# Kernel optimization log

Hardware: AMD Instinct MI355X
Metric: run time of the kernel (lower is better)

## Reference

```python
import jax, jax.numpy as jnp
import numpy as np

D_MODEL = 1024
N_HEADS = 16
D_HEAD = D_MODEL // N_HEADS
BLOCK = 2048
EPS = 1e-5


def layer_norm(x, w, b):
    mu = jnp.mean(x, axis=-1, keepdims=True)
    var = jnp.mean(jnp.square(x - mu), axis=-1, keepdims=True)
    return (x - mu) * jax.lax.rsqrt(var + EPS) * w + b


def setup_inputs() -> dict:
    key = jax.random.key(0)
    ks = jax.random.split(key, 8)
    d = D_MODEL
    s = 1.0 / np.sqrt(d)
    return {
        "x": jax.random.normal(ks[0], (2, 2048, d), dtype=jnp.float32),
        "ln1_w": jnp.ones((d,), jnp.float32),
        "ln1_b": jnp.zeros((d,), jnp.float32),
        "ln2_w": jnp.ones((d,), jnp.float32),
        "ln2_b": jnp.zeros((d,), jnp.float32),
        "qkv_w": jax.random.normal(ks[1], (3 * d, d), jnp.float32) * s,
        "o_w": jax.random.normal(ks[2], (d, d), jnp.float32) * s,
        "ffn_w1": jax.random.normal(ks[3], (4 * d, d), jnp.float32) * s,
        "ffn_b1": jnp.zeros((4 * d,), jnp.float32),
        "ffn_w2": jax.random.normal(ks[4], (d, 4 * d), jnp.float32) * (1.0 / np.sqrt(4 * d)),
        "ffn_b2": jnp.zeros((d,), jnp.float32),
    }


def reference(x, ln1_w, ln1_b, ln2_w, ln2_b, qkv_w, o_w, ffn_w1, ffn_b1, ffn_w2, ffn_b2):
    b, n, d = x.shape
    h = layer_norm(x, ln1_w, ln1_b)
    # qkv: (b, n, 3, H, Dh)
    qkv = (h @ qkv_w.T).reshape(b, n, 3, N_HEADS, D_HEAD)
    q, k, v = qkv[:, :, 0], qkv[:, :, 1], qkv[:, :, 2]  # (b, n, H, Dh)
    scale = 1.0 / np.sqrt(D_HEAD)
    s = jnp.einsum("bqhd,bkhd->bhqk", q, k) * scale
    mask = jnp.tril(jnp.ones((n, n), dtype=bool))
    s = jnp.where(mask, s, -jnp.inf)
    a = jax.nn.softmax(s, axis=-1)
    attn_out = jnp.einsum("bhqk,bkhd->bqhd", a, v).reshape(b, n, d)
    x = x + attn_out @ o_w.T
    h2 = layer_norm(x, ln2_w, ln2_b)
    ff = jax.nn.gelu(h2 @ ffn_w1.T + ffn_b1, approximate=False) @ ffn_w2.T + ffn_b2
    return x + ff
```

## Files before the change

kernel.cpp:

```cpp
#include <hip/hip_runtime.h>
#include <math.h>

#define D_MODEL 1024
#define N_HEADS 16
#define D_HEAD  64
#define SEQ     2048
#define BATCH   2
#define M_TOT   (BATCH*SEQ)
#define FFN_DIM 4096

typedef __attribute__((ext_vector_type(8))) short bf16x8;
typedef __attribute__((ext_vector_type(4))) float f32x4;
typedef __attribute__((ext_vector_type(8))) unsigned short u16x8;

__device__ __forceinline__ unsigned short f2bf(float f) {
  unsigned int u = __float_as_uint(f);
  return (unsigned short)((u + 0x7fffu + ((u >> 16) & 1u)) >> 16);
}
__device__ __forceinline__ unsigned short f2bf_trunc(float f) {
  return (unsigned short)(__float_as_uint(f) >> 16);
}
__device__ __forceinline__ float bf2f(unsigned short s) {
  return __uint_as_float(((unsigned int)s) << 16);
}

__device__ __forceinline__ void async_ld16(void* lds, const void* g) {
  __builtin_amdgcn_global_load_lds(
      (const __attribute__((address_space(1))) unsigned int*)g,
      (__attribute__((address_space(3))) unsigned int*)lds, 16, 0, 0);
}

__device__ __forceinline__ float gelu_exact(float x) {
  return 0.5f * x * (1.f + erff(x * 0.70710678118654752f));
}

__global__ __launch_bounds__(256) void cvt_all(const float* __restrict__ qkv_w,
    const float* __restrict__ o_w, const float* __restrict__ w1,
    const float* __restrict__ w2, unsigned short* __restrict__ dst) {
  const long MEGc = 1024*1024;
  long i = (long)(blockIdx.x*256 + threadIdx.x)*4;
  const float* src; long off;
  if (i < 3*MEGc)      { src = qkv_w; off = i; }
  else if (i < 4*MEGc) { src = o_w;  off = i - 3*MEGc; }
  else if (i < 8*MEGc) { src = w1;   off = i - 4*MEGc; }
  else                 { src = w2;   off = i - 8*MEGc; }
  float4 v = *(const float4*)(src + off);
  ushort4 o = { f2bf(v.x), f2bf(v.y), f2bf(v.z), f2bf(v.w) };
  *(ushort4*)(dst + i) = o;
}

__global__ __launch_bounds__(256) void ln_kernel(const float* __restrict__ x,
    const float* __restrict__ w, const float* __restrict__ b,
    unsigned short* __restrict__ out) {
  int row = blockIdx.x;
  const float* xr = x + (size_t)row * D_MODEL;
  int c = threadIdx.x * 4;
  float4 v = *(const float4*)(xr + c);
  float s = v.x + v.y + v.z + v.w;
  __shared__ float red[4];
  #pragma unroll
  for (int o = 32; o > 0; o >>= 1) s += __shfl_down(s, o, 64);
  int wave = threadIdx.x >> 6;
  if ((threadIdx.x & 63) == 0) red[wave] = s;
  __syncthreads();
  float mean = (red[0]+red[1]+red[2]+red[3]) * (1.f/D_MODEL);
  __syncthreads();
  float d0 = v.x-mean, d1 = v.y-mean, d2 = v.z-mean, d3 = v.w-mean;
  float s2 = d0*d0 + d1*d1 + d2*d2 + d3*d3;
  #pragma unroll
  for (int o = 32; o > 0; o >>= 1) s2 += __shfl_down(s2, o, 64);
  if ((threadIdx.x & 63) == 0) red[wave] = s2;
  __syncthreads();
  float var = (red[0]+red[1]+red[2]+red[3]) * (1.f/D_MODEL);
  float rs = rsqrtf(var + 1e-5f);
  float4 wv = *(const float4*)(w + c);
  float4 bv = *(const float4*)(b + c);
  ushort4 o = { f2bf(d0*rs*wv.x + bv.x), f2bf(d1*rs*wv.y + bv.y),
                f2bf(d2*rs*wv.z + bv.z), f2bf(d3*rs*wv.w + bv.w) };
  *(ushort4*)(out + (size_t)row*D_MODEL + c) = o;
}

__device__ __forceinline__ void swizzle_block(int nbx, int nby, int& bx, int& by) {
  int nb = nbx * nby;
  int bid = blockIdx.y * nbx + blockIdx.x;
  int chunk = nb >> 3;
  int bid2 = (bid & 7) * chunk + (bid >> 3);
  const int GM = 8;
  int ngroup = GM * nbx;
  int g = bid2 / ngroup, rem = bid2 % ngroup;
  by = g*GM + (rem % GM);
  bx = rem / GM;
}

template<int EPI, bool OBF, int BN>
__global__ __launch_bounds__(256) void gemm_mfma(
    const unsigned short* __restrict__ A, const unsigned short* __restrict__ Bt,
    float* __restrict__ Cf, unsigned short* __restrict__ Cb,
    const float* __restrict__ bias, const float* __restrict__ res,
    int M, int N, int K) {
  constexpr int BM = 128, BK = 32;
  constexpr int NI = (BN == 128) ? 4 : 2;
  __shared__ unsigned short As[2][BM*BK];
  __shared__ unsigned short Bs[2][BN*BK];
  int tid = threadIdx.x;
  int w = tid >> 6, l = tid & 63;
  int lg = l >> 4, lm = l & 15;
  int bx, by;
  swizzle_block(N/BN, M/BM, bx, by);
  int bm = by * BM, bn = bx * BN;
  int wm = (BN == 128) ? (w >> 1) * 64 : w * 32;
  int wn = (BN == 128) ? (w & 1) * 64 : 0;

  f32x4 acc[NI][4];
  #pragma unroll
  for (int i = 0; i < NI; ++i)
    #pragma unroll
    for (int j = 0; j < 4; ++j)
      acc[i][j] = (f32x4){0.f, 0.f, 0.f, 0.f};

  int fa0 = (2*w+0)*512 + l*8;
  int fa1 = (2*w+1)*512 + l*8;
  const unsigned short* a0 = A + (size_t)(bm + (fa0 >> 5))*K + (fa0 & 31);
  const unsigned short* a1 = A + (size_t)(bm + (fa1 >> 5))*K + (fa1 & 31);
  const unsigned short* b0;
  const unsigned short* b1 = nullptr;
  if (BN == 128) {
    b0 = Bt + (size_t)(bn + (fa0 >> 5))*K + (fa0 & 31);
    b1 = Bt + (size_t)(bn + (fa1 >> 5))*K + (fa1 & 31);
  } else {
    int fb0 = w*512 + l*8;
    b0 = Bt + (size_t)(bn + (fb0 >> 5))*K + (fb0 & 31);
  }

  auto stage = [&](int buf, int k0) {
    async_ld16(&As[buf][(2*w+0)*512], a0 + k0);
    async_ld16(&As[buf][(2*w+1)*512], a1 + k0);
    if (BN == 128) {
      async_ld16(&Bs[buf][(2*w+0)*512], b0 + k0);
      async_ld16(&Bs[buf][(2*w+1)*512], b1 + k0);
    } else {
      async_ld16(&Bs[buf][w*512], b0 + k0);
    }
  };

  int aoff = (wm + lm)*BK + lg*8;
  int boff = (wn + lm)*BK + lg*8;

  stage(0, 0);
  int niter = K / BK;
  for (int kt = 0; kt < niter; ++kt) {
    __syncthreads();
    if (kt + 1 < niter) stage((kt+1) & 1, (kt+1)*BK);
    int buf = kt & 1;
    bf16x8 af[NI], bfr[4];
    #pragma unroll
    for (int i = 0; i < NI; ++i) af[i]  = *(const bf16x8*)&As[buf][aoff + i*512];
    #pragma unroll
    for (int j = 0; j < 4; ++j)  bfr[j] = *(const bf16x8*)&Bs[buf][boff + j*512];
    #pragma unroll
    for (int i = 0; i < NI; ++i)
      #pragma unroll
      for (int j = 0; j < 4; ++j)
        acc[i][j] = __builtin_amdgcn_mfma_f32_16x16x32_bf16(af[i], bfr[j], acc[i][j], 0, 0, 0);
  }

  #pragma unroll
  for (int i = 0; i < NI; ++i) {
    #pragma unroll
    for (int j = 0; j < 4; ++j) {
      int col = bn + wn + j*16 + lm;
      #pragma unroll
      for (int r = 0; r < 4; ++r) {
        int row = bm + wm + i*16 + lg*4 + r;
        float v = acc[i][j][r];
        if (EPI == 1) v = gelu_exact(v + bias[col]);
        if (EPI == 2) v += res[(size_t)row*N + col];
        if (EPI == 3) v += bias[col] + res[(size_t)row*N + col];
        if (OBF) Cb[(size_t)row*N + col] = f2bf(v);
        else     Cf[(size_t)row*N + col] = v;
      }
    }
  }
}

__global__ __launch_bounds__(256) void vtrans_kernel(
    const unsigned short* __restrict__ qkvb, unsigned short* __restrict__ vT) {
  __shared__ unsigned short T[64*72];
  int nt = blockIdx.x, h = blockIdx.y, b = blockIdx.z;
  int tid = threadIdx.x;
  const unsigned short* vb = qkvb + (size_t)(b*SEQ)*(3*D_MODEL) + 2*D_MODEL + h*D_HEAD;
  #pragma unroll
  for (int it = 0; it < 2; ++it) {
    int idx = tid + it*256;
    int r = idx >> 3, c8 = (idx & 7)*8;
    *(u16x8*)&T[r*72 + c8] = *(const u16x8*)(vb + (size_t)(nt*64 + r)*(3*D_MODEL) + c8);
  }
  __syncthreads();
  unsigned short* vto = vT + ((size_t)(b*N_HEADS + h)*D_HEAD)*SEQ + nt*64;
  #pragma unroll
  for (int it = 0; it < 2; ++it) {
    int idx = tid + it*256;
    int d = idx >> 3, s8 = (idx & 7)*8;
    u16x8 o;
    #pragma unroll
    for (int i = 0; i < 8; ++i) o[i] = T[(s8+i)*72 + d];
    *(u16x8*)(vto + (size_t)d*SEQ + s8) = o;
  }
}

#define ATT_PAD 72
__device__ __forceinline__ void attn_step(
    const bf16x8* aq, float* m_i, float* l_i, f32x4* acc_o,
    const unsigned short* __restrict__ Ks, const unsigned short* __restrict__ Vt,
    unsigned short* __restrict__ pw, int lg, int lm, int qoff, bool diag) {
  f32x4 sacc[4];
  #pragma unroll
  for (int j = 0; j < 4; ++j) sacc[j] = (f32x4){0.f, 0.f, 0.f, 0.f};
  #pragma unroll
  for (int s = 0; s < 2; ++s)
    #pragma unroll
    for (int j = 0; j < 4; ++j)
      sacc[j] = __builtin_amdgcn_mfma_f32_16x16x32_bf16(
          aq[s], *(const bf16x8*)&Ks[(j*16+lm)*ATT_PAD + s*32 + lg*8], sacc[j], 0, 0, 0);
  if (diag) {
    #pragma unroll
    for (int j = 0; j < 4; ++j)
      #pragma unroll
      for (int r = 0; r < 4; ++r)
        if (j*16 + lm > qoff + lg*4 + r) sacc[j][r] = -INFINITY;
  }
  float alpha[4];
  #pragma unroll
  for (int r = 0; r < 4; ++r) {
    float rm = fmaxf(fmaxf(sacc[0][r], sacc[1][r]), fmaxf(sacc[2][r], sacc[3][r]));
    #pragma unroll
    for (int o = 1; o < 16; o <<= 1) rm = fmaxf(rm, __shfl_xor(rm, o));
    float mn = fmaxf(m_i[r], rm);
    alpha[r] = __expf(m_i[r] - mn);
    float rsum = 0.f;
    #pragma unroll
    for (int j = 0; j < 4; ++j) {
      float p = __expf(sacc[j][r] - mn);
      sacc[j][r] = p; rsum += p;
    }
    #pragma unroll
    for (int o = 1; o < 16; o <<= 1) rsum += __shfl_xor(rsum, o);
    l_i[r] = l_i[r]*alpha[r] + rsum;
    m_i[r] = mn;
  }
  #pragma unroll
  for (int j = 0; j < 4; ++j)
    #pragma unroll
    for (int r = 0; r < 4; ++r)
      pw[(lg*4 + r)*ATT_PAD + j*16 + lm] = f2bf_trunc(sacc[j][r]);
  #pragma unroll
  for (int j = 0; j < 4; ++j)
    #pragma unroll
    for (int r = 0; r < 4; ++r)
      acc_o[j][r] *= alpha[r];
  #pragma unroll
  for (int s = 0; s < 2; ++s) {
    bf16x8 ap = *(const bf16x8*)&pw[lm*ATT_PAD + s*32 + lg*8];
    #pragma unroll
    for (int j = 0; j < 4; ++j)
      acc_o[j] = __builtin_amdgcn_mfma_f32_16x16x32_bf16(
          ap, *(const bf16x8*)&Vt[(j*16+lm)*ATT_PAD + s*32 + lg*8], acc_o[j], 0, 0, 0);
  }
}

__global__ __launch_bounds__(256) void attn_mfma_kernel(
    const unsigned short* __restrict__ qkvb, const unsigned short* __restrict__ vT,
    unsigned short* __restrict__ out) {
  __shared__ unsigned short Ks[64*ATT_PAD];
  __shared__ unsigned short Vt[64*ATT_PAD];
  __shared__ unsigned short Pw[4][16*ATT_PAD];

  int pr = blockIdx.x, h = blockIdx.y, b = blockIdx.z;
  int qtH = 31 - pr, qtL = pr;
  int tid = threadIdx.x;
  int w = tid >> 6, l = tid & 63;
  int lg = l >> 4, lm = l & 15;

  const size_t rs3 = 3*D_MODEL;
  const unsigned short* qb  = qkvb + (size_t)(b*SEQ)*rs3 + h*D_HEAD;
  const unsigned short* kb  = qb + D_MODEL;
  const unsigned short* vtb = vT + ((size_t)(b*N_HEADS + h)*D_HEAD)*SEQ;

  bf16x8 aqH[2], aqL[2];
  int qrH = qtH*64 + w*16 + lm, qrL = qtL*64 + w*16 + lm;
  #pragma unroll
  for (int s = 0; s < 2; ++s) {
    u16x8 tH = *(const u16x8*)(qb + (size_t)qrH*rs3 + s*32 + lg*8);
    u16x8 tL = *(const u16x8*)(qb + (size_t)qrL*rs3 + s*32 + lg*8);
    bf16x8 rH, rL;
    #pragma unroll
    for (int i = 0; i < 8; ++i) {
      rH[i] = (short)f2bf(bf2f(tH[i]) * 0.125f);
      rL[i] = (short)f2bf(bf2f(tL[i]) * 0.125f);
    }
    aqH[s] = rH; aqL[s] = rL;
  }

  float mH[4], lH[4], mL[4], lL[4];
  f32x4 oH[4], oL[4];
  #pragma unroll
  for (int r = 0; r < 4; ++r) { mH[r] = -INFINITY; lH[r] = 0.f; mL[r] = -INFINITY; lL[r] = 0.f; }
  #pragma unroll
  for (int j = 0; j < 4; ++j) { oH[j] = (f32x4){0.f,0.f,0.f,0.f}; oL[j] = (f32x4){0.f,0.f,0.f,0.f}; }

  unsigned short* pw = &Pw[w][0];

  int sidx0 = tid, sidx1 = tid + 256;
  int sr0 = sidx0 >> 3, sc0 = (sidx0 & 7)*8;
  int sr1 = sidx1 >> 3, sc1 = (sidx1 & 7)*8;

  u16x8 kreg[2], vreg[2];
  auto prefetch = [&](int kt) {
    kreg[0] = *(const u16x8*)(kb  + (size_t)(kt*64 + sr0)*rs3 + sc0);
    kreg[1] = *(const u16x8*)(kb  + (size_t)(kt*64 + sr1)*rs3 + sc1);
    vreg[0] = *(const u16x8*)(vtb + (size_t)sr0*SEQ + kt*64 + sc0);
    vreg[1] = *(const u16x8*)(vtb + (size_t)sr1*SEQ + kt*64 + sc1);
  };

  prefetch(0);
  for (int kt = 0; kt <= qtH; ++kt) {
    __syncthreads();
    *(u16x8*)&Ks[sr0*ATT_PAD + sc0] = kreg[0];
    *(u16x8*)&Ks[sr1*ATT_PAD + sc1] = kreg[1];
    *(u16x8*)&Vt[sr0*ATT_PAD + sc0] = vreg[0];
    *(u16x8*)&Vt[sr1*ATT_PAD + sc1] = vreg[1];
    __syncthreads();
    if (kt < qtH) prefetch(kt+1);
    attn_step(aqH, mH, lH, oH, Ks, Vt, pw, lg, lm, w*16, kt == qtH);
    if (kt <= qtL)
      attn_step(aqL, mL, lL, oL, Ks, Vt, pw, lg, lm, w*16, kt == qtL);
  }

  #pragma unroll
  for (int r = 0; r < 4; ++r) {
    float invH = 1.f / lH[r], invL = 1.f / lL[r];
    int qH = qtH*64 + w*16 + lg*4 + r;
    int qL = qtL*64 + w*16 + lg*4 + r;
    #pragma unroll
    for (int j = 0; j < 4; ++j) {
      out[((size_t)(b*SEQ + qH))*D_MODEL + h*D_HEAD + j*16 + lm] = f2bf(oH[j][r]*invH);
      out[((size_t)(b*SEQ + qL))*D_MODEL + h*D_HEAD + j*16 + lm] = f2bf(oL[j][r]*invL);
    }
  }
}

extern "C" void kernel_launch(void* const* d_in, const int* in_sizes, int n_in,
                              void* d_out, int out_size, void* d_ws, size_t ws_size,
                              hipStream_t stream) {
  const float* x      = (const float*)d_in[0];
  const float* ln1_w  = (const float*)d_in[1];
  const float* ln1_b  = (const float*)d_in[2];
  const float* ln2_w  = (const float*)d_in[3];
  const float* ln2_b  = (const float*)d_in[4];
  const float* qkv_w  = (const float*)d_in[5];
  const float* o_w    = (const float*)d_in[6];
  const float* ffn_w1 = (const float*)d_in[7];
  const float* ffn_b1 = (const float*)d_in[8];
  const float* ffn_w2 = (const float*)d_in[9];
  const float* ffn_b2 = (const float*)d_in[10];
  float* out = (float*)d_out;
  float* ws  = (float*)d_ws;

  const size_t MEG = 1024*1024;
  unsigned short* wqkv = (unsigned short*)ws;
  unsigned short* wo   = wqkv + 3*MEG;
  unsigned short* w1   = wo   + 1*MEG;
  unsigned short* w2   = w1   + 4*MEG;
  unsigned short* hbf    = (unsigned short*)(ws + 6*MEG);
  unsigned short* attnbf = (unsigned short*)(ws + 8*MEG);
  float* x1  = ws + 10*MEG;
  unsigned short* qkvb = (unsigned short*)(ws + 14*MEG);
  unsigned short* ffbf = (unsigned short*)(ws + 14*MEG);
  unsigned short* vT   = (unsigned short*)(ws + 22*MEG);

  cvt_all<<<12*MEG/1024, 256, 0, stream>>>(qkv_w, o_w, ffn_w1, ffn_w2, wqkv);
  ln_kernel<<<M_TOT, 256, 0, stream>>>(x, ln1_w, ln1_b, hbf);
  gemm_mfma<0,true,128><<<dim3(3*D_MODEL/128, M_TOT/128), 256, 0, stream>>>(
      hbf, wqkv, nullptr, qkvb, nullptr, nullptr, M_TOT, 3*D_MODEL, D_MODEL);
  vtrans_kernel<<<dim3(SEQ/64, N_HEADS, BATCH), 256, 0, stream>>>(qkvb, vT);
  attn_mfma_kernel<<<dim3(16, N_HEADS, BATCH), 256, 0, stream>>>(qkvb, vT, attnbf);
  gemm_mfma<2,false,64><<<dim3(D_MODEL/64, M_TOT/128), 256, 0, stream>>>(
      attnbf, wo, x1, nullptr, nullptr, x, M_TOT, D_MODEL, D_MODEL);
  ln_kernel<<<M_TOT, 256, 0, stream>>>(x1, ln2_w, ln2_b, hbf);
  gemm_mfma<1,true,128><<<dim3(FFN_DIM/128, M_TOT/128), 256, 0, stream>>>(
      hbf, w1, nullptr, ffbf, ffn_b1, nullptr, M_TOT, FFN_DIM, D_MODEL);
  gemm_mfma<3,false,64><<<dim3(D_MODEL/64, M_TOT/128), 256, 0, stream>>>(
      ffbf, w2, out, nullptr, ffn_b2, x1, M_TOT, D_MODEL, FFN_DIM);
}
```

Before: 383.2 us.

## Shrink GEMM tiles to 64-row blocks with 2 waves and unified LDS staging

The GEMM kernel moves from 128-row tiles with 4 waves (256 threads) to 64-row tiles with 2 waves (128 threads). It also merges the A and B shared buffers into one staging array filled by a generic per-wave chunk loop. Each wave keeps the same per-wave MFMA tile. The grid doubles, which raises block count and can help wave scheduling and the tail across CUs. In exchange, B is reloaded from global memory twice as often per output, and each block has fewer waves to hide latency.

```diff
diff --git a/kernel.cpp b/kernel.cpp
--- a/kernel.cpp
+++ b/kernel.cpp
@@ -93,58 +93,51 @@
 }
 
 template<int EPI, bool OBF, int BN>
-__global__ __launch_bounds__(256) void gemm_mfma(
+__global__ __launch_bounds__(128) void gemm_mfma(
     const unsigned short* __restrict__ A, const unsigned short* __restrict__ Bt,
     float* __restrict__ Cf, unsigned short* __restrict__ Cb,
     const float* __restrict__ bias, const float* __restrict__ res,
     int M, int N, int K) {
-  constexpr int BM = 128, BK = 32;
-  constexpr int NI = (BN == 128) ? 4 : 2;
-  __shared__ unsigned short As[2][BM*BK];
-  __shared__ unsigned short Bs[2][BN*BK];
+  constexpr int BM = 64, BK = 32;
+  constexpr int TS = (BM + BN) * BK;
+  constexpr int CPW = TS / 1024;
+  constexpr int MI = (BN == 128) ? 4 : 2;
+  __shared__ unsigned short Ls[2][TS];
   int tid = threadIdx.x;
   int w = tid >> 6, l = tid & 63;
   int lg = l >> 4, lm = l & 15;
   int bx, by;
   swizzle_block(N/BN, M/BM, bx, by);
   int bm = by * BM, bn = bx * BN;
-  int wm = (BN == 128) ? (w >> 1) * 64 : w * 32;
-  int wn = (BN == 128) ? (w & 1) * 64 : 0;
-
-  f32x4 acc[NI][4];
-  #pragma unroll
-  for (int i = 0; i < NI; ++i)
+  int wm = (BN == 128) ? 0 : w*32;
+  int wn = (BN == 128) ? w*64 : 0;
+
+  f32x4 acc[MI][4];
+  #pragma unroll
+  for (int i = 0; i < MI; ++i)
     #pragma unroll
     for (int j = 0; j < 4; ++j)
       acc[i][j] = (f32x4){0.f, 0.f, 0.f, 0.f};
 
-  int fa0 = (2*w+0)*512 + l*8;
-  int fa1 = (2*w+1)*512 + l*8;
-  const unsigned short* a0 = A + (size_t)(bm + (fa0 >> 5))*K + (fa0 & 31);
-  const unsigned short* a1 = A + (size_t)(bm + (fa1 >> 5))*K + (fa1 & 31);
-  const unsigned short* b0;
-  const unsigned short* b1 = nullptr;
-  if (BN == 128) {
-    b0 = Bt + (size_t)(bn + (fa0 >> 5))*K + (fa0 & 31);
-    b1 = Bt + (size_t)(bn + (fa1 >> 5))*K + (fa1 & 31);
-  } else {
-    int fb0 = w*512 + l*8;
-    b0 = Bt + (size_t)(bn + (fb0 >> 5))*K + (fb0 & 31);
-  }
-
+  const unsigned short* gp[CPW];
+  int lo[CPW];
+  #pragma unroll
+  for (int cc = 0; cc < CPW; ++cc) {
+    int c = w*CPW + cc;
+    int r = c*16 + (l >> 2);
+    int col = (l & 3) * 8;
+    lo[cc] = c*512 + l*8;
+    gp[cc] = (r < BM) ? (A  + (size_t)(bm + r)*K + col)
+                      : (Bt + (size_t)(bn + (r - BM))*K + col);
+  }
   auto stage = [&](int buf, int k0) {
-    async_ld16(&As[buf][(2*w+0)*512], a0 + k0);
-    async_ld16(&As[buf][(2*w+1)*512], a1 + k0);
-    if (BN == 128) {
-      async_ld16(&Bs[buf][(2*w+0)*512], b0 + k0);
-      async_ld16(&Bs[buf][(2*w+1)*512], b1 + k0);
-    } else {
-      async_ld16(&Bs[buf][w*512], b0 + k0);
-    }
+    #pragma unroll
+    for (int cc = 0; cc < CPW; ++cc)
+      async_ld16(&Ls[buf][lo[cc]], gp[cc] + k0);
   };
 
   int aoff = (wm + lm)*BK + lg*8;
-  int boff = (wn + lm)*BK + lg*8;
+  int boff = BM*BK + (wn + lm)*BK + lg*8;
 
   stage(0, 0);
   int niter = K / BK;
@@ -152,20 +145,20 @@
     __syncthreads();
     if (kt + 1 < niter) stage((kt+1) & 1, (kt+1)*BK);
     int buf = kt & 1;
-    bf16x8 af[NI], bfr[4];
-    #pragma unroll
-    for (int i = 0; i < NI; ++i) af[i]  = *(const bf16x8*)&As[buf][aoff + i*512];
-    #pragma unroll
-    for (int j = 0; j < 4; ++j)  bfr[j] = *(const bf16x8*)&Bs[buf][boff + j*512];
-    #pragma unroll
-    for (int i = 0; i < NI; ++i)
+    bf16x8 af[MI], bfr[4];
+    #pragma unroll
+    for (int i = 0; i < MI; ++i) af[i]  = *(const bf16x8*)&Ls[buf][aoff + i*512];
+    #pragma unroll
+    for (int j = 0; j < 4; ++j)  bfr[j] = *(const bf16x8*)&Ls[buf][boff + j*512];
+    #pragma unroll
+    for (int i = 0; i < MI; ++i)
       #pragma unroll
       for (int j = 0; j < 4; ++j)
         acc[i][j] = __builtin_amdgcn_mfma_f32_16x16x32_bf16(af[i], bfr[j], acc[i][j], 0, 0, 0);
   }
 
   #pragma unroll
-  for (int i = 0; i < NI; ++i) {
+  for (int i = 0; i < MI; ++i) {
     #pragma unroll
     for (int j = 0; j < 4; ++j) {
       int col = bn + wn + j*16 + lm;
@@ -380,15 +373,15 @@
 
   cvt_all<<<12*MEG/1024, 256, 0, stream>>>(qkv_w, o_w, ffn_w1, ffn_w2, wqkv);
   ln_kernel<<<M_TOT, 256, 0, stream>>>(x, ln1_w, ln1_b, hbf);
-  gemm_mfma<0,true,128><<<dim3(3*D_MODEL/128, M_TOT/128), 256, 0, stream>>>(
+  gemm_mfma<0,true,128><<<dim3(3*D_MODEL/128, M_TOT/64), 128, 0, stream>>>(
       hbf, wqkv, nullptr, qkvb, nullptr, nullptr, M_TOT, 3*D_MODEL, D_MODEL);
   vtrans_kernel<<<dim3(SEQ/64, N_HEADS, BATCH), 256, 0, stream>>>(qkvb, vT);
   attn_mfma_kernel<<<dim3(16, N_HEADS, BATCH), 256, 0, stream>>>(qkvb, vT, attnbf);
-  gemm_mfma<2,false,64><<<dim3(D_MODEL/64, M_TOT/128), 256, 0, stream>>>(
+  gemm_mfma<2,false,64><<<dim3(D_MODEL/64, M_TOT/64), 128, 0, stream>>>(
       attnbf, wo, x1, nullptr, nullptr, x, M_TOT, D_MODEL, D_MODEL);
   ln_kernel<<<M_TOT, 256, 0, stream>>>(x1, ln2_w, ln2_b, hbf);
-  gemm_mfma<1,true,128><<<dim3(FFN_DIM/128, M_TOT/128), 256, 0, stream>>>(
+  gemm_mfma<1,true,128><<<dim3(FFN_DIM/128, M_TOT/64), 128, 0, stream>>>(
       hbf, w1, nullptr, ffbf, ffn_b1, nullptr, M_TOT, FFN_DIM, D_MODEL);
-  gemm_mfma<3,false,64><<<dim3(D_MODEL/64, M_TOT/128), 256, 0, stream>>>(
+  gemm_mfma<3,false,64><<<dim3(D_MODEL/64, M_TOT/64), 128, 0, stream>>>(
       ffbf, w2, out, nullptr, ffn_b2, x1, M_TOT, D_MODEL, FFN_DIM);
 }
```

Result: no change. 381.5 us (-0.5%).
